# Kernel tuning notes

Hardware: AMD Instinct MI355X
Metric: run time of the kernel (lower is better)

## Reference

```python
import jax, jax.numpy as jnp
import numpy as np

NQ = 4  # num_qubits
B = 131072
N_ACTIONS = 4


def _mat(a, b, c, d):
    # assemble (..., 2, 2) matrix from entries broadcast over leading dims
    return jnp.stack([jnp.stack([a, b], -1), jnp.stack([c, d], -1)], -2)


def _rx(t):
    c = jnp.cos(t / 2).astype(jnp.complex64)
    s = (-1j) * jnp.sin(t / 2).astype(jnp.complex64)
    return _mat(c, s, s, c)


def _ry(t):
    c = jnp.cos(t / 2).astype(jnp.complex64)
    s = jnp.sin(t / 2).astype(jnp.complex64)
    return _mat(c, -s, s, c)


def _rz(t):
    em = jnp.exp(-0.5j * t.astype(jnp.complex64))
    ep = jnp.exp(0.5j * t.astype(jnp.complex64))
    z = jnp.zeros_like(em)
    return _mat(em, z, z, ep)


def _apply_1q(psi, wire, U):
    # psi: (B,2,2,2,2), wire 0 is the most-significant axis (PennyLane order)
    psi = jnp.moveaxis(psi, 1 + wire, 1)
    if U.ndim == 2:
        psi = jnp.einsum('ij,bjklm->biklm', U, psi)
    else:  # per-sample gate, U: (B,2,2)
        psi = jnp.einsum('bij,bjklm->biklm', U, psi)
    return jnp.moveaxis(psi, 1, 1 + wire)


def _cnot(psi, c, t):
    psi = jnp.moveaxis(psi, (1 + c, 1 + t), (1, 2))
    # flip target where control == 1
    psi = jnp.concatenate([psi[:, :1], psi[:, 1:, ::-1]], axis=1)
    return jnp.moveaxis(psi, (1, 2), (1 + c, 1 + t))


# CNOT(wires=[(NQ-2-i)%NQ, (NQ-i-1)%NQ]) for i in 0..3
_CNOT_RING = [(2, 3), (1, 2), (0, 1), (3, 0)]


def _quantum_model(q_params, xe):
    # q_params: (32,), xe: (B,4) angles; returns (B,4) PauliZ expvals
    b = xe.shape[0]
    psi = jnp.zeros((b, 2, 2, 2, 2), jnp.complex64).at[:, 0, 0, 0, 0].set(1.0)
    for l in range(4):  # 4 embedding+ansatz blocks
        for w in range(NQ):
            psi = _apply_1q(psi, w, _rx(xe[:, w]))
        p = q_params[8 * l: 8 * (l + 1)]
        for w in range(NQ):
            psi = _apply_1q(psi, w, _ry(p[w]))
        for w in range(NQ):
            psi = _apply_1q(psi, w, _rz(p[NQ + w]))
        for c, t in _CNOT_RING:
            psi = _cnot(psi, c, t)
    probs = jnp.real(psi * jnp.conj(psi))  # (B,2,2,2,2) float32
    zdiag = jnp.array([1.0, -1.0], jnp.float32)
    evs = [jnp.sum(probs * zdiag.reshape((1,) + (1,) * w + (2,) + (1,) * (NQ - 1 - w)),
                   axis=(1, 2, 3, 4)) for w in range(NQ)]
    return jnp.stack(evs, axis=-1)


def setup_inputs() -> dict:
    key = jax.random.key(0)
    k0, k1, k2, k3 = jax.random.split(key, 4)
    x = jax.random.normal(k0, (B, NQ), jnp.float32)
    w_emb = jax.random.uniform(k1, (NQ,), jnp.float32, -1.0, 1.0)
    q_params = 0.1 * jax.random.normal(k2, (8 * NQ,), jnp.float32)
    W = jax.random.normal(k3, (N_ACTIONS, NQ), jnp.float32) / np.sqrt(NQ)
    b = jnp.zeros((N_ACTIONS,), jnp.float32)
    return {"x": x, "w_emb": w_emb, "q_params": q_params, "W": W, "b": b}


def reference(x, w_emb, q_params, W, b):
    xe = jnp.tanh(w_emb * x) * jnp.float32(np.pi)  # EncodingLayer
    xq = _quantum_model(q_params, xe)              # QuantumLayer, batched
    return jax.nn.relu(xq) @ W.T + b               # fc_out
```

## Files before the change

### kernel.cpp

```cpp
#include <hip/hip_runtime.h>
#include <math.h>

#define PI_F 3.14159265358979323846f

__device__ __forceinline__ float fast_tanh(float v) {
    float a = fabsf(v);
    float e = __expf(2.0f * a);
    float r = 1.0f - 2.0f * __builtin_amdgcn_rcpf(e + 1.0f);
    return copysignf(r, v);
}

__global__ __launch_bounds__(256) void qdqn_kernel(
    const float* __restrict__ x,
    const float* __restrict__ w_emb,
    const float* __restrict__ qp,
    const float* __restrict__ Wmat,
    const float* __restrict__ bias,
    float* __restrict__ out,
    int nbatch) {
    int b = blockIdx.x * 256 + threadIdx.x;
    if (b >= nbatch) return;

    const float4 xv = reinterpret_cast<const float4*>(x)[b];

    float cx[4], sx[4];
    {
        const float xs0 = xv.x, xs1 = xv.y, xs2 = xv.z, xs3 = xv.w;
        float a0 = 0.5f * PI_F * fast_tanh(w_emb[0] * xs0);
        float a1 = 0.5f * PI_F * fast_tanh(w_emb[1] * xs1);
        float a2 = 0.5f * PI_F * fast_tanh(w_emb[2] * xs2);
        float a3 = 0.5f * PI_F * fast_tanh(w_emb[3] * xs3);
        __sincosf(a0, &sx[0], &cx[0]);
        __sincosf(a1, &sx[1], &cx[1]);
        __sincosf(a2, &sx[2], &cx[2]);
        __sincosf(a3, &sx[3], &cx[3]);
    }

    float re[16], im[16];
    #pragma unroll
    for (int i = 0; i < 16; ++i) { re[i] = 0.0f; im[i] = 0.0f; }
    re[0] = 1.0f;

#define RX_GATE(W) { \
    const int pb = 3 - (W); const float c = cx[(W)], s = sx[(W)]; \
    _Pragma("unroll") \
    for (int i = 0; i < 16; ++i) { \
        if (((i >> pb) & 1) == 0) { \
            const int j = i | (1 << pb); \
            const float r0 = re[i], m0 = im[i], r1 = re[j], m1 = im[j]; \
            re[i] = fmaf(c, r0,  s * m1); \
            im[i] = fmaf(c, m0, -s * r1); \
            re[j] = fmaf(c, r1,  s * m0); \
            im[j] = fmaf(c, m1, -s * r0); \
        } } }

#define RY_GATE(W, C, S) { \
    const int pb = 3 - (W); const float c = (C), s = (S); \
    _Pragma("unroll") \
    for (int i = 0; i < 16; ++i) { \
        if (((i >> pb) & 1) == 0) { \
            const int j = i | (1 << pb); \
            const float r0 = re[i], m0 = im[i], r1 = re[j], m1 = im[j]; \
            re[i] = fmaf(c, r0, -s * r1); \
            im[i] = fmaf(c, m0, -s * m1); \
            re[j] = fmaf(s, r0,  c * r1); \
            im[j] = fmaf(s, m0,  c * m1); \
        } } }

#define RZ_GATE(W, C, S) { \
    const int pb = 3 - (W); const float c = (C), s = (S); \
    _Pragma("unroll") \
    for (int i = 0; i < 16; ++i) { \
        const float r = re[i], m = im[i]; \
        if ((i >> pb) & 1) { re[i] = fmaf(c, r, -s * m); im[i] = fmaf(c, m,  s * r); } \
        else               { re[i] = fmaf(c, r,  s * m); im[i] = fmaf(c, m, -s * r); } \
    } }

#define CNOT_GATE(C, T) { \
    const int pc = 3 - (C), pt = 3 - (T); \
    _Pragma("unroll") \
    for (int i = 0; i < 16; ++i) { \
        if (((i >> pc) & 1) && !((i >> pt) & 1)) { \
            const int j = i | (1 << pt); \
            const float tr = re[i]; re[i] = re[j]; re[j] = tr; \
            const float tm = im[i]; im[i] = im[j]; im[j] = tm; \
        } } }

    #pragma unroll
    for (int l = 0; l < 4; ++l) {
        RX_GATE(0) RX_GATE(1) RX_GATE(2) RX_GATE(3)

        const int o = 8 * l;
        float cq[8], sq[8];
        #pragma unroll
        for (int k = 0; k < 8; ++k) {
            __sincosf(0.5f * qp[o + k], &sq[k], &cq[k]);
        }

        RY_GATE(0, cq[0], sq[0])
        RY_GATE(1, cq[1], sq[1])
        RY_GATE(2, cq[2], sq[2])
        RY_GATE(3, cq[3], sq[3])

        RZ_GATE(0, cq[4], sq[4])
        RZ_GATE(1, cq[5], sq[5])
        RZ_GATE(2, cq[6], sq[6])
        RZ_GATE(3, cq[7], sq[7])

        CNOT_GATE(2, 3) CNOT_GATE(1, 2) CNOT_GATE(0, 1) CNOT_GATE(3, 0)
    }

    float p[16];
    #pragma unroll
    for (int i = 0; i < 16; ++i) p[i] = fmaf(re[i], re[i], im[i] * im[i]);

    float ev[4];
    #pragma unroll
    for (int w = 0; w < 4; ++w) {
        const int pb = 3 - w;
        float acc = 0.0f;
        #pragma unroll
        for (int i = 0; i < 16; ++i)
            acc += ((i >> pb) & 1) ? -p[i] : p[i];
        ev[w] = fmaxf(acc, 0.0f);
    }

    float4 o4;
    o4.x = fmaf(ev[0], Wmat[0],  fmaf(ev[1], Wmat[1],  fmaf(ev[2], Wmat[2],  fmaf(ev[3], Wmat[3],  bias[0]))));
    o4.y = fmaf(ev[0], Wmat[4],  fmaf(ev[1], Wmat[5],  fmaf(ev[2], Wmat[6],  fmaf(ev[3], Wmat[7],  bias[1]))));
    o4.z = fmaf(ev[0], Wmat[8],  fmaf(ev[1], Wmat[9],  fmaf(ev[2], Wmat[10], fmaf(ev[3], Wmat[11], bias[2]))));
    o4.w = fmaf(ev[0], Wmat[12], fmaf(ev[1], Wmat[13], fmaf(ev[2], Wmat[14], fmaf(ev[3], Wmat[15], bias[3]))));
    reinterpret_cast<float4*>(out)[b] = o4;
}

extern "C" void kernel_launch(void* const* d_in, const int* in_sizes, int n_in,
                              void* d_out, int out_size, void* d_ws, size_t ws_size,
                              hipStream_t stream) {
    const float* x     = (const float*)d_in[0];
    const float* w_emb = (const float*)d_in[1];
    const float* qp    = (const float*)d_in[2];
    const float* Wmat  = (const float*)d_in[3];
    const float* bias  = (const float*)d_in[4];
    float* out = (float*)d_out;

    const int nbatch = in_sizes[0] / 4;
    const int block = 256;
    const int grid = (nbatch + block - 1) / block;
    hipLaunchKernelGGL(qdqn_kernel, dim3(grid), dim3(block), 0, stream,
                       x, w_emb, qp, Wmat, bias, out, nbatch);
}
```

Measured before the change: 73.64 us.

## Fuse per-wire RX/RY/RZ into single SU2 gates and simplify first and last layers

Combines the RX, RY and RZ rotations on each wire into one precomputed SU(2) matrix applied in a single pass. The first layer is built directly as a product state from the |0000> input. The last layer drops RZ, which does not change Z probabilities, and the final CNOT ring is folded into XOR-parity signs in the expectation sum. This removes many per-amplitude FMAs and register shuffles, at the cost of extra per-thread trig setup and algebra that is harder to verify.

```diff
diff --git a/kernel.cpp b/kernel.cpp
--- a/kernel.cpp
+++ b/kernel.cpp
@@ -9,6 +9,29 @@
     float r = 1.0f - 2.0f * __builtin_amdgcn_rcpf(e + 1.0f);
     return copysignf(r, v);
 }
+
+#define SU2_GATE(W, AR, AI, BR, BI) { \
+    const float Ar_ = (AR), Ai_ = (AI), Br_ = (BR), Bi_ = (BI); \
+    _Pragma("unroll") \
+    for (int i_ = 0; i_ < 16; ++i_) { \
+        if (((i_ >> (3 - (W))) & 1) == 0) { \
+            const int j_ = i_ | (1 << (3 - (W))); \
+            const float a0r = re[i_], a0i = im[i_], a1r = re[j_], a1i = im[j_]; \
+            re[i_] = fmaf(Ar_, a0r, fmaf(-Ai_, a0i, fmaf(-Br_, a1r, -Bi_ * a1i))); \
+            im[i_] = fmaf(Ar_, a0i, fmaf( Ai_, a0r, fmaf(-Br_, a1i,  Bi_ * a1r))); \
+            re[j_] = fmaf(Br_, a0r, fmaf(-Bi_, a0i, fmaf( Ar_, a1r,  Ai_ * a1i))); \
+            im[j_] = fmaf(Br_, a0i, fmaf( Bi_, a0r, fmaf( Ar_, a1i, -Ai_ * a1r))); \
+        } } }
+
+#define CNOT_GATE(C, T) { \
+    const int pc_ = 3 - (C), pt_ = 3 - (T); \
+    _Pragma("unroll") \
+    for (int i_ = 0; i_ < 16; ++i_) { \
+        if (((i_ >> pc_) & 1) && !((i_ >> pt_) & 1)) { \
+            const int j_ = i_ | (1 << pt_); \
+            const float tr_ = re[i_]; re[i_] = re[j_]; re[j_] = tr_; \
+            const float tm_ = im[i_]; im[i_] = im[j_]; im[j_] = tm_; \
+        } } }
 
 __global__ __launch_bounds__(256) void qdqn_kernel(
     const float* __restrict__ x,
@@ -25,11 +48,10 @@
 
     float cx[4], sx[4];
     {
-        const float xs0 = xv.x, xs1 = xv.y, xs2 = xv.z, xs3 = xv.w;
-        float a0 = 0.5f * PI_F * fast_tanh(w_emb[0] * xs0);
-        float a1 = 0.5f * PI_F * fast_tanh(w_emb[1] * xs1);
-        float a2 = 0.5f * PI_F * fast_tanh(w_emb[2] * xs2);
-        float a3 = 0.5f * PI_F * fast_tanh(w_emb[3] * xs3);
+        float a0 = 0.5f * PI_F * fast_tanh(w_emb[0] * xv.x);
+        float a1 = 0.5f * PI_F * fast_tanh(w_emb[1] * xv.y);
+        float a2 = 0.5f * PI_F * fast_tanh(w_emb[2] * xv.z);
+        float a3 = 0.5f * PI_F * fast_tanh(w_emb[3] * xv.w);
         __sincosf(a0, &sx[0], &cx[0]);
         __sincosf(a1, &sx[1], &cx[1]);
         __sincosf(a2, &sx[2], &cx[2]);
@@ -37,77 +59,67 @@
     }
 
     float re[16], im[16];
-    #pragma unroll
-    for (int i = 0; i < 16; ++i) { re[i] = 0.0f; im[i] = 0.0f; }
-    re[0] = 1.0f;
 
-#define RX_GATE(W) { \
-    const int pb = 3 - (W); const float c = cx[(W)], s = sx[(W)]; \
-    _Pragma("unroll") \
-    for (int i = 0; i < 16; ++i) { \
-        if (((i >> pb) & 1) == 0) { \
-            const int j = i | (1 << pb); \
-            const float r0 = re[i], m0 = im[i], r1 = re[j], m1 = im[j]; \
-            re[i] = fmaf(c, r0,  s * m1); \
-            im[i] = fmaf(c, m0, -s * r1); \
-            re[j] = fmaf(c, r1,  s * m0); \
-            im[j] = fmaf(c, m1, -s * r0); \
-        } } }
-
-#define RY_GATE(W, C, S) { \
-    const int pb = 3 - (W); const float c = (C), s = (S); \
-    _Pragma("unroll") \
-    for (int i = 0; i < 16; ++i) { \
-        if (((i >> pb) & 1) == 0) { \
-            const int j = i | (1 << pb); \
-            const float r0 = re[i], m0 = im[i], r1 = re[j], m1 = im[j]; \
-            re[i] = fmaf(c, r0, -s * r1); \
-            im[i] = fmaf(c, m0, -s * m1); \
-            re[j] = fmaf(s, r0,  c * r1); \
-            im[j] = fmaf(s, m0,  c * m1); \
-        } } }
-
-#define RZ_GATE(W, C, S) { \
-    const int pb = 3 - (W); const float c = (C), s = (S); \
-    _Pragma("unroll") \
-    for (int i = 0; i < 16; ++i) { \
-        const float r = re[i], m = im[i]; \
-        if ((i >> pb) & 1) { re[i] = fmaf(c, r, -s * m); im[i] = fmaf(c, m,  s * r); } \
-        else               { re[i] = fmaf(c, r,  s * m); im[i] = fmaf(c, m, -s * r); } \
-    } }
-
-#define CNOT_GATE(C, T) { \
-    const int pc = 3 - (C), pt = 3 - (T); \
-    _Pragma("unroll") \
-    for (int i = 0; i < 16; ++i) { \
-        if (((i >> pc) & 1) && !((i >> pt) & 1)) { \
-            const int j = i | (1 << pt); \
-            const float tr = re[i]; re[i] = re[j]; re[j] = tr; \
-            const float tm = im[i]; im[i] = im[j]; im[j] = tm; \
-        } } }
+    {
+        float pr[4][2], pim[4][2];
+        #pragma unroll
+        for (int w = 0; w < 4; ++w) {
+            float cy, sy, cz, sz;
+            __sincosf(0.5f * qp[w],     &sy, &cy);
+            __sincosf(0.5f * qp[4 + w], &sz, &cz);
+            const float v0r = cy * cx[w], v0i = sy * sx[w];
+            const float v1r = sy * cx[w], v1i = -(cy * sx[w]);
+            pr[w][0]  = fmaf(v0r, cz,  v0i * sz);
+            pim[w][0] = fmaf(v0i, cz, -v0r * sz);
+            pr[w][1]  = fmaf(v1r, cz, -v1i * sz);
+            pim[w][1] = fmaf(v1i, cz,  v1r * sz);
+        }
+        float t01r[4], t01i[4], t23r[4], t23i[4];
+        #pragma unroll
+        for (int a = 0; a < 2; ++a)
+            #pragma unroll
+            for (int c = 0; c < 2; ++c) {
+                const int k = a * 2 + c;
+                t01r[k] = fmaf(pr[0][a], pr[1][c], -pim[0][a] * pim[1][c]);
+                t01i[k] = fmaf(pr[0][a], pim[1][c], pim[0][a] * pr[1][c]);
+                t23r[k] = fmaf(pr[2][a], pr[3][c], -pim[2][a] * pim[3][c]);
+                t23i[k] = fmaf(pr[2][a], pim[3][c], pim[2][a] * pr[3][c]);
+            }
+        #pragma unroll
+        for (int i = 0; i < 16; ++i) {
+            const int hi = i >> 2, lo = i & 3;
+            re[i] = fmaf(t01r[hi], t23r[lo], -t01i[hi] * t23i[lo]);
+            im[i] = fmaf(t01r[hi], t23i[lo],  t01i[hi] * t23r[lo]);
+        }
+    }
+    CNOT_GATE(2, 3) CNOT_GATE(1, 2) CNOT_GATE(0, 1) CNOT_GATE(3, 0)
 
     #pragma unroll
-    for (int l = 0; l < 4; ++l) {
-        RX_GATE(0) RX_GATE(1) RX_GATE(2) RX_GATE(3)
+    for (int l = 1; l <= 2; ++l) {
+        const int o = 8 * l;
+        #pragma unroll
+        for (int w = 0; w < 4; ++w) {
+            float cy, sy, cz, sz;
+            __sincosf(0.5f * qp[o + w],     &sy, &cy);
+            __sincosf(0.5f * qp[o + 4 + w], &sz, &cz);
+            const float ar = cy * cx[w], ai = sy * sx[w];
+            const float br = sy * cx[w], bi = -(cy * sx[w]);
+            const float Ar = fmaf(ar, cz,  ai * sz);
+            const float Ai = fmaf(ai, cz, -ar * sz);
+            const float Br = fmaf(br, cz, -bi * sz);
+            const float Bi = fmaf(bi, cz,  br * sz);
+            SU2_GATE(w, Ar, Ai, Br, Bi)
+        }
+        CNOT_GATE(2, 3) CNOT_GATE(1, 2) CNOT_GATE(0, 1) CNOT_GATE(3, 0)
+    }
 
-        const int o = 8 * l;
-        float cq[8], sq[8];
-        #pragma unroll
-        for (int k = 0; k < 8; ++k) {
-            __sincosf(0.5f * qp[o + k], &sq[k], &cq[k]);
-        }
-
-        RY_GATE(0, cq[0], sq[0])
-        RY_GATE(1, cq[1], sq[1])
-        RY_GATE(2, cq[2], sq[2])
-        RY_GATE(3, cq[3], sq[3])
-
-        RZ_GATE(0, cq[4], sq[4])
-        RZ_GATE(1, cq[5], sq[5])
-        RZ_GATE(2, cq[6], sq[6])
-        RZ_GATE(3, cq[7], sq[7])
-
-        CNOT_GATE(2, 3) CNOT_GATE(1, 2) CNOT_GATE(0, 1) CNOT_GATE(3, 0)
+    #pragma unroll
+    for (int w = 0; w < 4; ++w) {
+        float cy, sy;
+        __sincosf(0.5f * qp[24 + w], &sy, &cy);
+        const float Ar = cy * cx[w], Ai = sy * sx[w];
+        const float Br = sy * cx[w], Bi = -(cy * sx[w]);
+        SU2_GATE(w, Ar, Ai, Br, Bi)
     }
 
     float p[16];
@@ -117,11 +129,17 @@
     float ev[4];
     #pragma unroll
     for (int w = 0; w < 4; ++w) {
-        const int pb = 3 - w;
         float acc = 0.0f;
         #pragma unroll
-        for (int i = 0; i < 16; ++i)
-            acc += ((i >> pb) & 1) ? -p[i] : p[i];
+        for (int i = 0; i < 16; ++i) {
+            const int a0 = (i >> 3) & 1, a1 = (i >> 2) & 1, a2 = (i >> 1) & 1, a3 = i & 1;
+            int s;
+            if (w == 0)      s = a0 ^ a2 ^ a3;
+            else if (w == 1) s = a0 ^ a1;
+            else if (w == 2) s = a1 ^ a2;
+            else             s = a2 ^ a3;
+            acc += s ? -p[i] : p[i];
+        }
         ev[w] = fmaxf(acc, 0.0f);
     }
 
```

Result: faster. 69.40 us (-5.8%).
